# Performance work log

Hardware: AMD Instinct MI355X
Metric: run time of the kernel (lower is better)

## Reference

```python
import jax, jax.numpy as jnp
import numpy as np

N = 50000          # nodes
E = 800000         # edges per metapath
P = 4              # metapaths
IN = 256           # in_size
D = 32 * 8         # out_size * layer_num_heads = 256
SEM_H = 128        # SemanticAttention hidden


def setup_inputs() -> dict:
    key = jax.random.key(0)
    ks = jax.random.split(key, 8)
    h = jax.random.normal(ks[0], (N, IN), dtype=jnp.float32)
    src = jax.random.randint(ks[1], (P, E), 0, N, dtype=jnp.int32)
    dst = jax.random.randint(ks[2], (P, E), 0, N, dtype=jnp.int32)
    # per-metapath GraphConv weights (Glorot-ish scale)
    W_gc = jax.random.normal(ks[3], (P, IN, D), dtype=jnp.float32) / np.sqrt(IN)
    b_gc = jnp.zeros((P, D), dtype=jnp.float32)
    # SemanticAttention: Linear(D, SEM_H) -> tanh -> Linear(SEM_H, 1, bias=False)
    W1 = jax.random.normal(ks[4], (D, SEM_H), dtype=jnp.float32) / np.sqrt(D)
    b1 = jnp.zeros((SEM_H,), dtype=jnp.float32)
    w2 = jax.random.normal(ks[5], (SEM_H,), dtype=jnp.float32) / np.sqrt(SEM_H)
    return {"h": h, "src": src, "dst": dst, "W_gc": W_gc, "b_gc": b_gc,
            "W1": W1, "b1": b1, "w2": w2}


def _graph_conv(h, src, dst, W, b):
    # DGL GraphConv with norm='both': D_dst^{-1/2} A D_src^{-1/2} (h W) + b
    ones = jnp.ones((src.shape[0],), dtype=h.dtype)
    deg_out = jnp.clip(jax.ops.segment_sum(ones, src, num_segments=N), 1.0)
    deg_in = jnp.clip(jax.ops.segment_sum(ones, dst, num_segments=N), 1.0)
    x = (h @ W) * jax.lax.rsqrt(deg_out)[:, None]          # [N, D]
    agg = jax.ops.segment_sum(x[src], dst, num_segments=N)  # gather-scatter [N, D]
    return agg * jax.lax.rsqrt(deg_in)[:, None] + b


def reference(h, src, dst, W_gc, b_gc, W1, b1, w2):
    # per-metapath GraphConv (fixed small loop over P metapaths)
    zs = [_graph_conv(h, src[p], dst[p], W_gc[p], b_gc[p]) for p in range(P)]
    z = jnp.stack(zs, axis=1)                               # [N, P, D]
    # SemanticAttention: project -> mean over nodes -> softmax over metapaths
    s = jnp.tanh(z @ W1 + b1) @ w2                          # [N, P]
    beta = jax.nn.softmax(s.mean(axis=0), axis=0)           # [P]
    return jnp.einsum('npd,p->nd', z, beta)                 # [N, D]
```

## Files before the change

### kernel.cpp

```cpp
#include <hip/hip_runtime.h>

#define NN 50000
#define NE 800000
#define NP 4
#define DIN 256
#define DD 256
#define NH 128
#define SA 40
#define NSEG 16
#define SEGE (NE / NSEG)
#define HCH 16384
#define NHC 4
#define SCH 8192
#define NSC 7
#define SPAD(k) ((k) + ((k) >> 5))

typedef __attribute__((ext_vector_type(8))) short bf16x8;
typedef __attribute__((ext_vector_type(4))) float f32x4;
typedef __attribute__((ext_vector_type(2))) float f32x2;

__device__ __forceinline__ unsigned short f2bf(float f) {
  unsigned u = __float_as_uint(f);
  u += 0x7fff + ((u >> 16) & 1);
  return (unsigned short)(u >> 16);
}

__device__ __forceinline__ f32x2 unpk(unsigned u) {
  f32x2 f;
  f.x = __uint_as_float(u << 16);
  f.y = __uint_as_float(u & 0xffff0000u);
  return f;
}
__device__ __forceinline__ void pkfma(f32x2& acc, f32x2 m, f32x2 v) {
  asm("v_pk_fma_f32 %0, %1, %2, %0" : "+v"(acc) : "v"(m), "v"(v));
}


__global__ __launch_bounds__(256) void hist2d_kernel(const int* __restrict__ idx,
                                                     int* __restrict__ cnt) {
  int bx = blockIdx.x;
  int c = bx % NHC, s = bx / NHC;
  int p = blockIdx.y;
  int base = c * HCH, nk = min(HCH, NN - base);
  __shared__ int hs[HCH];
  for (int k = threadIdx.x; k < HCH; k += 256) hs[k] = 0;
  __syncthreads();
  const int4* a4 = (const int4*)(idx + (size_t)p * NE + (size_t)s * SEGE);
  for (int i = threadIdx.x; i < SEGE / 4; i += 256) {
    int4 v = a4[i];
    int k;
    k = v.x - base; if ((unsigned)k < (unsigned)nk) atomicAdd(&hs[k], 1);
    k = v.y - base; if ((unsigned)k < (unsigned)nk) atomicAdd(&hs[k], 1);
    k = v.z - base; if ((unsigned)k < (unsigned)nk) atomicAdd(&hs[k], 1);
    k = v.w - base; if ((unsigned)k < (unsigned)nk) atomicAdd(&hs[k], 1);
  }
  __syncthreads();
  int* out = cnt + (size_t)(p * NSEG + s) * NN + base;
  for (int k = threadIdx.x; k < nk; k += 256) out[k] = hs[k];
}


__global__ __launch_bounds__(1024) void scanA_kernel(
    int* __restrict__ cntD, const int* __restrict__ cntS,
    float* __restrict__ rin, float* __restrict__ rout,
    int* __restrict__ row_ptr, int* __restrict__ chunkdeg) {
  int c = blockIdx.x, p = blockIdx.y;
  int base = c * SCH, nk = min(SCH, NN - base);
  __shared__ int sdeg[SCH + (SCH >> 5)];
  __shared__ int wtot[16], wexc[16];
  int t = threadIdx.x;
  for (int kk = t; kk < SCH; kk += 1024) {
    int run = 0;
    if (kk < nk) {
      size_t o = (size_t)(p * NSEG) * NN + base + kk;
      for (int s = 0; s < NSEG; ++s) {
        size_t oo = o + (size_t)s * NN;
        int v = cntD[oo];
        cntD[oo] = run;
        run += v;
      }
      rin[(size_t)p * NN + base + kk] = rsqrtf((float)max(run, 1));
      int rs = 0;
      for (int s = 0; s < NSEG; ++s) rs += cntS[o + (size_t)s * NN];
      rout[(size_t)p * NN + base + kk] = rsqrtf((float)max(rs, 1));
    }
    sdeg[SPAD(kk)] = run;
  }
  __syncthreads();
  int loc[8];
  int ssum = 0;
#pragma unroll
  for (int j = 0; j < 8; ++j) { loc[j] = ssum; ssum += sdeg[SPAD(t * 8 + j)]; }
  int incl = ssum;
  int lane = t & 63, w = t >> 6;
#pragma unroll
  for (int o = 1; o < 64; o <<= 1) {
    int v = __shfl_up(incl, o);
    if (lane >= o) incl += v;
  }
  if (lane == 63) wtot[w] = incl;
  __syncthreads();
  if (t == 0) {
    int r = 0;
    for (int i = 0; i < 16; ++i) { wexc[i] = r; r += wtot[i]; }
  }
  __syncthreads();
  int tbase = wexc[w] + incl - ssum;
  int* rp = row_ptr + (size_t)p * (NN + 1) + base;
#pragma unroll
  for (int j = 0; j < 8; ++j) {
    int k = t * 8 + j;
    if (k < nk) rp[k] = tbase + loc[j];
  }
  if (t == 1023) chunkdeg[p * NSC + c] = tbase + ssum;
}


__global__ void scanB_kernel(const int* __restrict__ chunkdeg, int* __restrict__ chunk_base,
                             int* __restrict__ row_ptr) {
  int t = threadIdx.x;
  if (t < NP) {
    int run = 0;
    for (int c = 0; c < NSC; ++c) { chunk_base[t * NSC + c] = run; run += chunkdeg[t * NSC + c]; }
    row_ptr[(size_t)t * (NN + 1) + NN] = NE;
  }
}

__global__ __launch_bounds__(1024) void rpfin_kernel(int* __restrict__ row_ptr,
                                                     const int* __restrict__ chunk_base) {
  int k = blockIdx.x * 1024 + threadIdx.x, p = blockIdx.y;
  if (k < NN) row_ptr[(size_t)p * (NN + 1) + k] += chunk_base[p * NSC + (k >> 13)];
}


__global__ __launch_bounds__(256) void scatter_kernel(
    const int* __restrict__ src, const int* __restrict__ dst,
    const int* __restrict__ cntD, const int* __restrict__ row_ptr, int* __restrict__ col) {
  int bx = blockIdx.x;
  int c = bx % NHC, s = bx / NHC;
  int p = blockIdx.y;
  int base = c * HCH, nk = min(HCH, NN - base);
  __shared__ int cur[HCH];
  for (int k = threadIdx.x; k < nk; k += 256)
    cur[k] = row_ptr[(size_t)p * (NN + 1) + base + k] +
             cntD[(size_t)(p * NSEG + s) * NN + base + k];
  __syncthreads();
  const int4* d4 = (const int4*)(dst + (size_t)p * NE + (size_t)s * SEGE);
  const int4* s4 = (const int4*)(src + (size_t)p * NE + (size_t)s * SEGE);
  int* colp = col + (size_t)p * NE;
  for (int i = threadIdx.x; i < SEGE / 4; i += 256) {
    int4 dv = d4[i];
    int4 sv = s4[i];
    int k;
    k = dv.x - base; if ((unsigned)k < (unsigned)nk) colp[atomicAdd(&cur[k], 1)] = sv.x;
    k = dv.y - base; if ((unsigned)k < (unsigned)nk) colp[atomicAdd(&cur[k], 1)] = sv.y;
    k = dv.z - base; if ((unsigned)k < (unsigned)nk) colp[atomicAdd(&cur[k], 1)] = sv.z;
    k = dv.w - base; if ((unsigned)k < (unsigned)nk) colp[atomicAdd(&cur[k], 1)] = sv.w;
  }
}


__global__ void cvt_h_kernel(const float4* __restrict__ h4, ushort4* __restrict__ h2) {
  int i = blockIdx.x * blockDim.x + threadIdx.x;
  if (i >= NN * DIN / 4) return;
  float4 v = h4[i];
  ushort4 o;
  o.x = f2bf(v.x); o.y = f2bf(v.y); o.z = f2bf(v.z); o.w = f2bf(v.w);
  h2[i] = o;
}


__global__ __launch_bounds__(256) void agg_kernel(
    const ushort* __restrict__ h2, const int* __restrict__ col,
    const int* __restrict__ row_ptr, const float* __restrict__ rout,
    const float* __restrict__ rin, ushort* __restrict__ g) {
  __shared__ int2 sW[4][64];
  int p = blockIdx.y;
  int v = blockIdx.x * 4 + (threadIdx.x >> 6);
  int lane = threadIdx.x & 63;
  int wv = threadIdx.x >> 6;
  const int* colp = col + (size_t)p * NE;
  const float* rop = rout + (size_t)p * NN;
  int beg = row_ptr[p * (NN + 1) + v], end = row_ptr[p * (NN + 1) + v + 1];
  const char* hb = (const char*)h2 + (size_t)lane * 8;
  f32x2 accA0 = {0.f, 0.f}, accA1 = {0.f, 0.f};
  f32x2 accB0 = {0.f, 0.f}, accB1 = {0.f, 0.f};
  for (int j0 = beg; j0 < end; j0 += 64) {
    int nw = end - j0;
    if (nw > 64) nw = 64;
    int cv = 0;
    float rv = 0.f;
    if (lane < nw) { cv = colp[j0 + lane]; rv = rop[cv]; }
    sW[wv][lane] = make_int2(cv, __float_as_int(rv));
    int nwb = (nw + 7) & ~7;
    for (int t = 0; t < nwb; t += 8) {
      int2 w[8];
#pragma unroll
      for (int q = 0; q < 8; ++q) w[q] = sW[wv][t + q];
      uint2 u[8];
#pragma unroll
      for (int q = 0; q < 8; ++q)
        u[q] = *(const uint2*)(hb + ((size_t)(unsigned)w[q].x << 9));
#pragma unroll
      for (int q = 0; q < 8; ++q) {
        float r = __int_as_float(w[q].y);
        f32x2 rr = {r, r};
        if (q & 1) {
          pkfma(accB0, rr, unpk(u[q].x));
          pkfma(accB1, rr, unpk(u[q].y));
        } else {
          pkfma(accA0, rr, unpk(u[q].x));
          pkfma(accA1, rr, unpk(u[q].y));
        }
      }
    }
  }
  float ri = rin[(size_t)p * NN + v];
  f32x2 s0 = accA0 + accB0;
  f32x2 s1 = accA1 + accB1;
  ushort4 o;
  o.x = f2bf(s0.x * ri); o.y = f2bf(s0.y * ri);
  o.z = f2bf(s1.x * ri); o.w = f2bf(s1.y * ri);
  ((ushort4*)(g + ((size_t)p * NN + v) * DIN))[lane] = o;
}


__global__ void wmul_kernel(const float* __restrict__ Wgc, const float* __restrict__ W1,
                            ushort* __restrict__ Mt) {
  int p = blockIdx.y, k = blockIdx.x, j = threadIdx.x;
  const float* wrow = Wgc + ((size_t)p * DIN + k) * DD;
  float s = 0.f;
  for (int d = 0; d < DD; ++d) s = fmaf(wrow[d], W1[(size_t)d * NH + j], s);
  Mt[((size_t)p * NH + j) * DIN + k] = f2bf(s);
}

__global__ void cvec_kernel(const float* __restrict__ bgc, const float* __restrict__ W1,
                            const float* __restrict__ b1, float* __restrict__ cvec) {
  int p = blockIdx.x, j = threadIdx.x;
  const float* b = bgc + (size_t)p * DD;
  float s = b1[j];
  for (int d = 0; d < DD; ++d) s = fmaf(b[d], W1[(size_t)d * NH + j], s);
  cvec[p * NH + j] = s;
}


__global__ __launch_bounds__(256) void gemm_sem(
    const ushort* __restrict__ g, const ushort* __restrict__ Mt,
    const float* __restrict__ cvec, const float* __restrict__ w2,
    float* __restrict__ ssum) {
  __shared__ ushort As[128 * SA];
  __shared__ ushort Bs[128 * SA];
  __shared__ float wsumf[4];
  const int tid = threadIdx.x;
  const int p = blockIdx.y;
  const int row0 = blockIdx.x * 128;
  const int wave = tid >> 6, lane = tid & 63;
  const int wr = wave >> 1, wc = wave & 1;
  const int srow = tid >> 2, sseg = tid & 3;
  const int fr = lane & 15, fk = (lane >> 4) * 8;
  const ushort* Ag = g + (size_t)p * NN * DIN;
  const ushort* Bg = Mt + (size_t)p * NH * DIN;
  int ar0 = row0 + srow; if (ar0 >= NN) ar0 = NN - 1;
  int ar1 = row0 + srow + 64; if (ar1 >= NN) ar1 = NN - 1;
  f32x4 acc[4][4] = {};
  for (int k2 = 0; k2 < DIN; k2 += 32) {
    uint4 av0 = *(const uint4*)(Ag + (size_t)ar0 * DIN + k2 + sseg * 8);
    uint4 av1 = *(const uint4*)(Ag + (size_t)ar1 * DIN + k2 + sseg * 8);
    uint4 bv0 = *(const uint4*)(Bg + (size_t)srow * DIN + k2 + sseg * 8);
    uint4 bv1 = *(const uint4*)(Bg + (size_t)(srow + 64) * DIN + k2 + sseg * 8);
    __syncthreads();
    *(uint4*)&As[srow * SA + sseg * 8] = av0;
    *(uint4*)&As[(srow + 64) * SA + sseg * 8] = av1;
    *(uint4*)&Bs[srow * SA + sseg * 8] = bv0;
    *(uint4*)&Bs[(srow + 64) * SA + sseg * 8] = bv1;
    __syncthreads();
    bf16x8 af[4], bfv[4];
#pragma unroll
    for (int t = 0; t < 4; ++t) {
      af[t] = *(const bf16x8*)&As[(wr * 64 + t * 16 + fr) * SA + fk];
      bfv[t] = *(const bf16x8*)&Bs[(wc * 64 + t * 16 + fr) * SA + fk];
    }
#pragma unroll
    for (int mt = 0; mt < 4; ++mt)
#pragma unroll
      for (int nt = 0; nt < 4; ++nt)
        acc[mt][nt] = __builtin_amdgcn_mfma_f32_16x16x32_bf16(af[mt], bfv[nt], acc[mt][nt], 0, 0, 0);
  }
  float s = 0.f;
#pragma unroll
  for (int nt = 0; nt < 4; ++nt) {
    int c = wc * 64 + nt * 16 + fr;
    float cc = cvec[p * NH + c];
    float ww = w2[c];
#pragma unroll
    for (int mt = 0; mt < 4; ++mt)
#pragma unroll
      for (int i = 0; i < 4; ++i) {
        int r = row0 + wr * 64 + mt * 16 + (lane >> 4) * 4 + i;
        if (r < NN) {
          float x = acc[mt][nt][i] + cc;
          x = fminf(fmaxf(x, -15.f), 15.f);
          float e = __expf(2.f * x);
          s = fmaf((e - 1.f) / (e + 1.f), ww, s);
        }
      }
  }
#pragma unroll
  for (int o = 32; o > 0; o >>= 1) s += __shfl_down(s, o);
  if (lane == 0) wsumf[wave] = s;
  __syncthreads();
  if (tid == 0) atomicAdd(&ssum[p], wsumf[0] + wsumf[1] + wsumf[2] + wsumf[3]);
}


__global__ void beta_kernel(const float* __restrict__ ssum, const float* __restrict__ bgc,
                            float* __restrict__ beta, float* __restrict__ bout) {
  __shared__ float sb[NP];
  if (threadIdx.x == 0) {
    float m[NP];
    float mx = -1e30f;
    for (int p = 0; p < NP; ++p) {
      m[p] = ssum[p] / (float)NN;
      mx = fmaxf(mx, m[p]);
    }
    float tot = 0.f;
    for (int p = 0; p < NP; ++p) { m[p] = expf(m[p] - mx); tot += m[p]; }
    for (int p = 0; p < NP; ++p) { sb[p] = m[p] / tot; beta[p] = sb[p]; }
  }
  __syncthreads();
  int d = threadIdx.x;
  float s = 0.f;
  for (int p = 0; p < NP; ++p) s = fmaf(sb[p], bgc[p * DD + d], s);
  bout[d] = s;
}

__global__ void scaleWt_kernel(const float* __restrict__ Wgc, const float* __restrict__ beta,
                               ushort* __restrict__ Wt) {
  int i = blockIdx.x * blockDim.x + threadIdx.x;
  if (i >= DD * NP * DIN) return;
  int n = i >> 10;
  int pk = i & 1023;
  int p = pk >> 8, k = pk & 255;
  Wt[i] = f2bf(beta[p] * Wgc[((size_t)p * DIN + k) * DD + n]);
}


__global__ __launch_bounds__(256) void gemm_main(
    const ushort* __restrict__ g, const ushort* __restrict__ Wt,
    const float* __restrict__ bout, float* __restrict__ out) {
  __shared__ ushort As[128 * SA];
  __shared__ ushort Bs[128 * SA];
  const int tid = threadIdx.x;
  const int row0 = blockIdx.y * 128;
  const int col0 = blockIdx.x * 128;
  const int wave = tid >> 6, lane = tid & 63;
  const int wr = wave >> 1, wc = wave & 1;
  const int srow = tid >> 2, sseg = tid & 3;
  const int fr = lane & 15, fk = (lane >> 4) * 8;
  int ar0 = row0 + srow; if (ar0 >= NN) ar0 = NN - 1;
  int ar1 = row0 + srow + 64; if (ar1 >= NN) ar1 = NN - 1;
  f32x4 acc[4][4] = {};
  for (int p = 0; p < NP; ++p) {
    const ushort* Ag = g + (size_t)p * NN * DIN;
    for (int k2 = 0; k2 < DIN; k2 += 32) {
      uint4 av0 = *(const uint4*)(Ag + (size_t)ar0 * DIN + k2 + sseg * 8);
      uint4 av1 = *(const uint4*)(Ag + (size_t)ar1 * DIN + k2 + sseg * 8);
      uint4 bv0 = *(const uint4*)(Wt + (size_t)(col0 + srow) * (NP * DIN) + p * DIN + k2 + sseg * 8);
      uint4 bv1 = *(const uint4*)(Wt + (size_t)(col0 + srow + 64) * (NP * DIN) + p * DIN + k2 + sseg * 8);
      __syncthreads();
      *(uint4*)&As[srow * SA + sseg * 8] = av0;
      *(uint4*)&As[(srow + 64) * SA + sseg * 8] = av1;
      *(uint4*)&Bs[srow * SA + sseg * 8] = bv0;
      *(uint4*)&Bs[(srow + 64) * SA + sseg * 8] = bv1;
      __syncthreads();
      bf16x8 af[4], bfv[4];
#pragma unroll
      for (int t = 0; t < 4; ++t) {
        af[t] = *(const bf16x8*)&As[(wr * 64 + t * 16 + fr) * SA + fk];
        bfv[t] = *(const bf16x8*)&Bs[(wc * 64 + t * 16 + fr) * SA + fk];
      }
#pragma unroll
      for (int mt = 0; mt < 4; ++mt)
#pragma unroll
        for (int nt = 0; nt < 4; ++nt)
          acc[mt][nt] = __builtin_amdgcn_mfma_f32_16x16x32_bf16(af[mt], bfv[nt], acc[mt][nt], 0, 0, 0);
    }
  }
#pragma unroll
  for (int nt = 0; nt < 4; ++nt) {
    int c = col0 + wc * 64 + nt * 16 + fr;
    float bb = bout[c];
#pragma unroll
    for (int mt = 0; mt < 4; ++mt)
#pragma unroll
      for (int i = 0; i < 4; ++i) {
        int r = row0 + wr * 64 + mt * 16 + (lane >> 4) * 4 + i;
        if (r < NN) out[(size_t)r * DD + c] = acc[mt][nt][i] + bb;
      }
  }
}


extern "C" void kernel_launch(void* const* d_in, const int* in_sizes, int n_in,
                              void* d_out, int out_size, void* d_ws, size_t ws_size,
                              hipStream_t stream) {
  const float* h = (const float*)d_in[0];
  const int* src = (const int*)d_in[1];
  const int* dst = (const int*)d_in[2];
  const float* Wgc = (const float*)d_in[3];
  const float* bgc = (const float*)d_in[4];
  const float* W1 = (const float*)d_in[5];
  const float* b1 = (const float*)d_in[6];
  const float* w2 = (const float*)d_in[7];
  float* out = (float*)d_out;

  char* base = (char*)d_ws;
  size_t off = 0;
  auto alloc = [&](size_t bytes) -> char* {
    char* ptr = base + off;
    off = (off + bytes + 255) & ~(size_t)255;
    return ptr;
  };
  int* cntD = (int*)alloc((size_t)NP * NSEG * NN * sizeof(int));
  int* cntS = (int*)alloc((size_t)NP * NSEG * NN * sizeof(int));
  float* rin = (float*)alloc((size_t)NP * NN * sizeof(float));
  float* rout = (float*)alloc((size_t)NP * NN * sizeof(float));
  int* row_ptr = (int*)alloc((size_t)NP * (NN + 1) * sizeof(int));
  int* chunkdeg = (int*)alloc((size_t)NP * NSC * sizeof(int));
  int* chunk_base = (int*)alloc((size_t)NP * NSC * sizeof(int));
  ushort* h2 = (ushort*)alloc((size_t)NN * DIN * sizeof(ushort));
  ushort* g = (ushort*)alloc((size_t)NP * NN * DIN * sizeof(ushort));
  ushort* Mt = (ushort*)alloc((size_t)NP * NH * DIN * sizeof(ushort));
  ushort* Wt = (ushort*)alloc((size_t)DD * NP * DIN * sizeof(ushort));
  float* cvec = (float*)alloc((size_t)NP * NH * sizeof(float));
  float* ssum = (float*)alloc(NP * sizeof(float));
  float* beta = (float*)alloc(NP * sizeof(float));
  float* bout = (float*)alloc(DD * sizeof(float));
  int* colbuf = (int*)cntS;
  if (off > ws_size) return;

  hipMemsetAsync(ssum, 0, NP * sizeof(float), stream);

  hist2d_kernel<<<dim3(NHC * NSEG, NP), 256, 0, stream>>>(dst, cntD);
  hist2d_kernel<<<dim3(NHC * NSEG, NP), 256, 0, stream>>>(src, cntS);
  scanA_kernel<<<dim3(NSC, NP), 1024, 0, stream>>>(cntD, cntS, rin, rout, row_ptr, chunkdeg);
  scanB_kernel<<<1, 64, 0, stream>>>(chunkdeg, chunk_base, row_ptr);
  rpfin_kernel<<<dim3((NN + 1023) / 1024, NP), 1024, 0, stream>>>(row_ptr, chunk_base);
  cvt_h_kernel<<<(NN * DIN / 4 + 255) / 256, 256, 0, stream>>>((const float4*)h, (ushort4*)h2);
  scatter_kernel<<<dim3(NHC * NSEG, NP), 256, 0, stream>>>(src, dst, cntD, row_ptr, colbuf);
  agg_kernel<<<dim3(NN / 4, NP), 256, 0, stream>>>(h2, colbuf, row_ptr, rout, rin, g);
  wmul_kernel<<<dim3(DIN, NP), NH, 0, stream>>>(Wgc, W1, Mt);
  cvec_kernel<<<NP, NH, 0, stream>>>(bgc, W1, b1, cvec);
  gemm_sem<<<dim3((NN + 127) / 128, NP), 256, 0, stream>>>(g, Mt, cvec, w2, ssum);
  beta_kernel<<<1, 256, 0, stream>>>(ssum, bgc, beta, bout);
  scaleWt_kernel<<<(DD * NP * DIN + 255) / 256, 256, 0, stream>>>(Wgc, beta, Wt);
  gemm_main<<<dim3(2, (NN + 127) / 128), 256, 0, stream>>>(g, Wt, bout, out);
}
```

Baseline: 631.0 us.

## Precompute edge weights in CSR scatter and widen aggregation gathers to 16 bytes

The scatter kernel now stores each edge as an (src, rsqrt out-degree) pair, so the aggregation kernel no longer does a dependent gather of rout per edge. The aggregation kernel splits each wavefront into two halves that each process alternate edges, loading 16-byte rows per lane, and then combines the halves with a cross-lane shuffle. This removes one level of indirect loads and makes memory accesses wider. In exchange it needs an extra 8-byte-per-edge buffer instead of reusing cntS, does more random reads of rout in the scatter, and adds a shuffle reduction at the end.

```diff
diff --git a/kernel.cpp b/kernel.cpp
--- a/kernel.cpp
+++ b/kernel.cpp
@@ -23,6 +23,9 @@
   unsigned u = __float_as_uint(f);
   u += 0x7fff + ((u >> 16) & 1);
   return (unsigned short)(u >> 16);
+}
+__device__ __forceinline__ unsigned pk2(float a, float b) {
+  return (unsigned)f2bf(a) | ((unsigned)f2bf(b) << 16);
 }
 
 __device__ __forceinline__ f32x2 unpk(unsigned u) {
@@ -135,7 +138,8 @@
 
 __global__ __launch_bounds__(256) void scatter_kernel(
     const int* __restrict__ src, const int* __restrict__ dst,
-    const int* __restrict__ cntD, const int* __restrict__ row_ptr, int* __restrict__ col) {
+    const int* __restrict__ cntD, const int* __restrict__ row_ptr,
+    const float* __restrict__ rout, int2* __restrict__ col2) {
   int bx = blockIdx.x;
   int c = bx % NHC, s = bx / NHC;
   int p = blockIdx.y;
@@ -147,15 +151,32 @@
   __syncthreads();
   const int4* d4 = (const int4*)(dst + (size_t)p * NE + (size_t)s * SEGE);
   const int4* s4 = (const int4*)(src + (size_t)p * NE + (size_t)s * SEGE);
-  int* colp = col + (size_t)p * NE;
+  const float* rop = rout + (size_t)p * NN;
+  int2* colp = col2 + (size_t)p * NE;
   for (int i = threadIdx.x; i < SEGE / 4; i += 256) {
     int4 dv = d4[i];
     int4 sv = s4[i];
     int k;
-    k = dv.x - base; if ((unsigned)k < (unsigned)nk) colp[atomicAdd(&cur[k], 1)] = sv.x;
-    k = dv.y - base; if ((unsigned)k < (unsigned)nk) colp[atomicAdd(&cur[k], 1)] = sv.y;
-    k = dv.z - base; if ((unsigned)k < (unsigned)nk) colp[atomicAdd(&cur[k], 1)] = sv.z;
-    k = dv.w - base; if ((unsigned)k < (unsigned)nk) colp[atomicAdd(&cur[k], 1)] = sv.w;
+    k = dv.x - base;
+    if ((unsigned)k < (unsigned)nk) {
+      float wv = rop[sv.x];
+      colp[atomicAdd(&cur[k], 1)] = make_int2(sv.x, __float_as_int(wv));
+    }
+    k = dv.y - base;
+    if ((unsigned)k < (unsigned)nk) {
+      float wv = rop[sv.y];
+      colp[atomicAdd(&cur[k], 1)] = make_int2(sv.y, __float_as_int(wv));
+    }
+    k = dv.z - base;
+    if ((unsigned)k < (unsigned)nk) {
+      float wv = rop[sv.z];
+      colp[atomicAdd(&cur[k], 1)] = make_int2(sv.z, __float_as_int(wv));
+    }
+    k = dv.w - base;
+    if ((unsigned)k < (unsigned)nk) {
+      float wv = rop[sv.w];
+      colp[atomicAdd(&cur[k], 1)] = make_int2(sv.w, __float_as_int(wv));
+    }
   }
 }
 
@@ -171,57 +192,59 @@
 
 
 __global__ __launch_bounds__(256) void agg_kernel(
-    const ushort* __restrict__ h2, const int* __restrict__ col,
-    const int* __restrict__ row_ptr, const float* __restrict__ rout,
+    const ushort* __restrict__ h2, const int2* __restrict__ col2,
+    const int* __restrict__ row_ptr,
     const float* __restrict__ rin, ushort* __restrict__ g) {
   __shared__ int2 sW[4][64];
   int p = blockIdx.y;
   int v = blockIdx.x * 4 + (threadIdx.x >> 6);
   int lane = threadIdx.x & 63;
   int wv = threadIdx.x >> 6;
-  const int* colp = col + (size_t)p * NE;
-  const float* rop = rout + (size_t)p * NN;
+  const int2* colp = col2 + (size_t)p * NE;
   int beg = row_ptr[p * (NN + 1) + v], end = row_ptr[p * (NN + 1) + v + 1];
-  const char* hb = (const char*)h2 + (size_t)lane * 8;
-  f32x2 accA0 = {0.f, 0.f}, accA1 = {0.f, 0.f};
-  f32x2 accB0 = {0.f, 0.f}, accB1 = {0.f, 0.f};
+  const uint4* h4 = (const uint4*)h2;
+  int half = lane >> 5;
+  int l32 = lane & 31;
+  f32x2 acc0 = {0.f, 0.f}, acc1 = {0.f, 0.f}, acc2 = {0.f, 0.f}, acc3 = {0.f, 0.f};
   for (int j0 = beg; j0 < end; j0 += 64) {
     int nw = end - j0;
     if (nw > 64) nw = 64;
-    int cv = 0;
-    float rv = 0.f;
-    if (lane < nw) { cv = colp[j0 + lane]; rv = rop[cv]; }
-    sW[wv][lane] = make_int2(cv, __float_as_int(rv));
-    int nwb = (nw + 7) & ~7;
-    for (int t = 0; t < nwb; t += 8) {
+    int2 wp = make_int2(0, 0);
+    if (lane < nw) wp = colp[j0 + lane];
+    sW[wv][lane] = wp;
+    int nwb = (nw + 15) & ~15;
+    for (int t = 0; t < nwb; t += 16) {
       int2 w[8];
 #pragma unroll
-      for (int q = 0; q < 8; ++q) w[q] = sW[wv][t + q];
-      uint2 u[8];
+      for (int q = 0; q < 8; ++q) w[q] = sW[wv][t + 2 * q + half];
+      uint4 u[8];
 #pragma unroll
       for (int q = 0; q < 8; ++q)
-        u[q] = *(const uint2*)(hb + ((size_t)(unsigned)w[q].x << 9));
+        u[q] = h4[((unsigned)w[q].x << 5) + l32];
 #pragma unroll
       for (int q = 0; q < 8; ++q) {
         float r = __int_as_float(w[q].y);
         f32x2 rr = {r, r};
-        if (q & 1) {
-          pkfma(accB0, rr, unpk(u[q].x));
-          pkfma(accB1, rr, unpk(u[q].y));
-        } else {
-          pkfma(accA0, rr, unpk(u[q].x));
-          pkfma(accA1, rr, unpk(u[q].y));
-        }
+        pkfma(acc0, rr, unpk(u[q].x));
+        pkfma(acc1, rr, unpk(u[q].y));
+        pkfma(acc2, rr, unpk(u[q].z));
+        pkfma(acc3, rr, unpk(u[q].w));
       }
     }
   }
+  acc0.x += __shfl_xor(acc0.x, 32); acc0.y += __shfl_xor(acc0.y, 32);
+  acc1.x += __shfl_xor(acc1.x, 32); acc1.y += __shfl_xor(acc1.y, 32);
+  acc2.x += __shfl_xor(acc2.x, 32); acc2.y += __shfl_xor(acc2.y, 32);
+  acc3.x += __shfl_xor(acc3.x, 32); acc3.y += __shfl_xor(acc3.y, 32);
   float ri = rin[(size_t)p * NN + v];
-  f32x2 s0 = accA0 + accB0;
-  f32x2 s1 = accA1 + accB1;
-  ushort4 o;
-  o.x = f2bf(s0.x * ri); o.y = f2bf(s0.y * ri);
-  o.z = f2bf(s1.x * ri); o.w = f2bf(s1.y * ri);
-  ((ushort4*)(g + ((size_t)p * NN + v) * DIN))[lane] = o;
+  if (half == 0) {
+    uint4 o;
+    o.x = pk2(acc0.x * ri, acc0.y * ri);
+    o.y = pk2(acc1.x * ri, acc1.y * ri);
+    o.z = pk2(acc2.x * ri, acc2.y * ri);
+    o.w = pk2(acc3.x * ri, acc3.y * ri);
+    ((uint4*)(g + ((size_t)p * NN + v) * DIN))[l32] = o;
+  }
 }
 
 
@@ -436,7 +459,7 @@
   float* ssum = (float*)alloc(NP * sizeof(float));
   float* beta = (float*)alloc(NP * sizeof(float));
   float* bout = (float*)alloc(DD * sizeof(float));
-  int* colbuf = (int*)cntS;
+  int2* col2 = (int2*)alloc((size_t)NP * NE * sizeof(int2));
   if (off > ws_size) return;
 
   hipMemsetAsync(ssum, 0, NP * sizeof(float), stream);
@@ -447,8 +470,8 @@
   scanB_kernel<<<1, 64, 0, stream>>>(chunkdeg, chunk_base, row_ptr);
   rpfin_kernel<<<dim3((NN + 1023) / 1024, NP), 1024, 0, stream>>>(row_ptr, chunk_base);
   cvt_h_kernel<<<(NN * DIN / 4 + 255) / 256, 256, 0, stream>>>((const float4*)h, (ushort4*)h2);
-  scatter_kernel<<<dim3(NHC * NSEG, NP), 256, 0, stream>>>(src, dst, cntD, row_ptr, colbuf);
-  agg_kernel<<<dim3(NN / 4, NP), 256, 0, stream>>>(h2, colbuf, row_ptr, rout, rin, g);
+  scatter_kernel<<<dim3(NHC * NSEG, NP), 256, 0, stream>>>(src, dst, cntD, row_ptr, rout, col2);
+  agg_kernel<<<dim3(NN / 4, NP), 256, 0, stream>>>(h2, col2, row_ptr, rin, g);
   wmul_kernel<<<dim3(DIN, NP), NH, 0, stream>>>(Wgc, W1, Mt);
   cvec_kernel<<<NP, NH, 0, stream>>>(bgc, W1, b1, cvec);
   gemm_sem<<<dim3((NN + 127) / 128, NP), 256, 0, stream>>>(g, Mt, cvec, w2, ssum);
```

Measured after the change: 659.1 us. 1.04x slower.

## Widen main GEMM tile to full output width and fuse small setup kernels

Applied to the files above, without the earlier changes.

The main GEMM now has each block compute all 256 output columns for 128 rows, so the large g operand is read from memory once instead of twice. This doubles the accumulator registers per thread and the B tile in shared memory, which may reduce occupancy. The weight-product and bias-vector kernels are merged into one launch, and the softmax/beta step is folded into the weight scaling kernel, removing two launches. The aggregation inner loop is only rewritten inline with no change in behaviour.

```diff
diff --git a/kernel.cpp b/kernel.cpp
--- a/kernel.cpp
+++ b/kernel.cpp
@@ -24,16 +24,8 @@
   u += 0x7fff + ((u >> 16) & 1);
   return (unsigned short)(u >> 16);
 }
-
-__device__ __forceinline__ f32x2 unpk(unsigned u) {
-  f32x2 f;
-  f.x = __uint_as_float(u << 16);
-  f.y = __uint_as_float(u & 0xffff0000u);
-  return f;
-}
-__device__ __forceinline__ void pkfma(f32x2& acc, f32x2 m, f32x2 v) {
-  asm("v_pk_fma_f32 %0, %1, %2, %0" : "+v"(acc) : "v"(m), "v"(v));
-}
+__device__ __forceinline__ float bfl(unsigned u) { return __uint_as_float(u << 16); }
+__device__ __forceinline__ float bfh(unsigned u) { return __uint_as_float(u & 0xffff0000u); }
 
 
 __global__ __launch_bounds__(256) void hist2d_kernel(const int* __restrict__ idx,
@@ -206,11 +198,11 @@
         float r = __int_as_float(w[q].y);
         f32x2 rr = {r, r};
         if (q & 1) {
-          pkfma(accB0, rr, unpk(u[q].x));
-          pkfma(accB1, rr, unpk(u[q].y));
+          asm("v_pk_fma_f32 %0, %1, %2, %0" : "+v"(accB0) : "v"(rr), "v"((f32x2){bfl(u[q].x), bfh(u[q].x)}));
+          asm("v_pk_fma_f32 %0, %1, %2, %0" : "+v"(accB1) : "v"(rr), "v"((f32x2){bfl(u[q].y), bfh(u[q].y)}));
         } else {
-          pkfma(accA0, rr, unpk(u[q].x));
-          pkfma(accA1, rr, unpk(u[q].y));
+          asm("v_pk_fma_f32 %0, %1, %2, %0" : "+v"(accA0) : "v"(rr), "v"((f32x2){bfl(u[q].x), bfh(u[q].x)}));
+          asm("v_pk_fma_f32 %0, %1, %2, %0" : "+v"(accA1) : "v"(rr), "v"((f32x2){bfl(u[q].y), bfh(u[q].y)}));
         }
       }
     }
@@ -225,22 +217,21 @@
 }
 
 
-__global__ void wmul_kernel(const float* __restrict__ Wgc, const float* __restrict__ W1,
-                            ushort* __restrict__ Mt) {
+__global__ void wmulcvec_kernel(const float* __restrict__ Wgc, const float* __restrict__ bgc,
+                                const float* __restrict__ W1, const float* __restrict__ b1,
+                                ushort* __restrict__ Mt, float* __restrict__ cvec) {
   int p = blockIdx.y, k = blockIdx.x, j = threadIdx.x;
-  const float* wrow = Wgc + ((size_t)p * DIN + k) * DD;
-  float s = 0.f;
-  for (int d = 0; d < DD; ++d) s = fmaf(wrow[d], W1[(size_t)d * NH + j], s);
-  Mt[((size_t)p * NH + j) * DIN + k] = f2bf(s);
-}
-
-__global__ void cvec_kernel(const float* __restrict__ bgc, const float* __restrict__ W1,
-                            const float* __restrict__ b1, float* __restrict__ cvec) {
-  int p = blockIdx.x, j = threadIdx.x;
-  const float* b = bgc + (size_t)p * DD;
-  float s = b1[j];
-  for (int d = 0; d < DD; ++d) s = fmaf(b[d], W1[(size_t)d * NH + j], s);
-  cvec[p * NH + j] = s;
+  if (k < DIN) {
+    const float* wrow = Wgc + ((size_t)p * DIN + k) * DD;
+    float s = 0.f;
+    for (int d = 0; d < DD; ++d) s = fmaf(wrow[d], W1[(size_t)d * NH + j], s);
+    Mt[((size_t)p * NH + j) * DIN + k] = f2bf(s);
+  } else {
+    const float* b = bgc + (size_t)p * DD;
+    float s = b1[j];
+    for (int d = 0; d < DD; ++d) s = fmaf(b[d], W1[(size_t)d * NH + j], s);
+    cvec[p * NH + j] = s;
+  }
 }
 
 
@@ -313,35 +304,36 @@
 }
 
 
-__global__ void beta_kernel(const float* __restrict__ ssum, const float* __restrict__ bgc,
-                            float* __restrict__ beta, float* __restrict__ bout) {
-  __shared__ float sb[NP];
-  if (threadIdx.x == 0) {
-    float m[NP];
-    float mx = -1e30f;
-    for (int p = 0; p < NP; ++p) {
-      m[p] = ssum[p] / (float)NN;
-      mx = fmaxf(mx, m[p]);
-    }
-    float tot = 0.f;
-    for (int p = 0; p < NP; ++p) { m[p] = expf(m[p] - mx); tot += m[p]; }
-    for (int p = 0; p < NP; ++p) { sb[p] = m[p] / tot; beta[p] = sb[p]; }
-  }
-  __syncthreads();
-  int d = threadIdx.x;
-  float s = 0.f;
-  for (int p = 0; p < NP; ++p) s = fmaf(sb[p], bgc[p * DD + d], s);
-  bout[d] = s;
-}
-
-__global__ void scaleWt_kernel(const float* __restrict__ Wgc, const float* __restrict__ beta,
-                               ushort* __restrict__ Wt) {
-  int i = blockIdx.x * blockDim.x + threadIdx.x;
-  if (i >= DD * NP * DIN) return;
-  int n = i >> 10;
-  int pk = i & 1023;
-  int p = pk >> 8, k = pk & 255;
-  Wt[i] = f2bf(beta[p] * Wgc[((size_t)p * DIN + k) * DD + n]);
+__global__ __launch_bounds__(256) void scaleWtB_kernel(const float* __restrict__ Wgc,
+                                                       const float* __restrict__ ssum,
+                                                       const float* __restrict__ bgc,
+                                                       ushort* __restrict__ Wt,
+                                                       float* __restrict__ bout) {
+  float m[NP];
+  float mx = -1e30f;
+#pragma unroll
+  for (int p = 0; p < NP; ++p) {
+    m[p] = ssum[p] * (1.f / (float)NN);
+    mx = fmaxf(mx, m[p]);
+  }
+  float tot = 0.f;
+#pragma unroll
+  for (int p = 0; p < NP; ++p) { m[p] = __expf(m[p] - mx); tot += m[p]; }
+  float inv = 1.f / tot;
+  if (blockIdx.x == 0) {
+    int d = threadIdx.x;
+    float s = 0.f;
+#pragma unroll
+    for (int p = 0; p < NP; ++p) s = fmaf(m[p] * inv, bgc[p * DD + d], s);
+    bout[d] = s;
+  }
+  int i = blockIdx.x * 256 + threadIdx.x;
+  if (i < DD * NP * DIN) {
+    int n = i >> 10;
+    int pk = i & 1023;
+    int p = pk >> 8, k = pk & 255;
+    Wt[i] = f2bf(m[p] * inv * Wgc[((size_t)p * DIN + k) * DD + n]);
+  }
 }
 
 
@@ -349,46 +341,50 @@
     const ushort* __restrict__ g, const ushort* __restrict__ Wt,
     const float* __restrict__ bout, float* __restrict__ out) {
   __shared__ ushort As[128 * SA];
-  __shared__ ushort Bs[128 * SA];
+  __shared__ ushort Bs[256 * SA];
   const int tid = threadIdx.x;
-  const int row0 = blockIdx.y * 128;
-  const int col0 = blockIdx.x * 128;
+  const int row0 = blockIdx.x * 128;
   const int wave = tid >> 6, lane = tid & 63;
   const int wr = wave >> 1, wc = wave & 1;
   const int srow = tid >> 2, sseg = tid & 3;
   const int fr = lane & 15, fk = (lane >> 4) * 8;
   int ar0 = row0 + srow; if (ar0 >= NN) ar0 = NN - 1;
   int ar1 = row0 + srow + 64; if (ar1 >= NN) ar1 = NN - 1;
-  f32x4 acc[4][4] = {};
+  f32x4 acc[4][8] = {};
   for (int p = 0; p < NP; ++p) {
     const ushort* Ag = g + (size_t)p * NN * DIN;
     for (int k2 = 0; k2 < DIN; k2 += 32) {
       uint4 av0 = *(const uint4*)(Ag + (size_t)ar0 * DIN + k2 + sseg * 8);
       uint4 av1 = *(const uint4*)(Ag + (size_t)ar1 * DIN + k2 + sseg * 8);
-      uint4 bv0 = *(const uint4*)(Wt + (size_t)(col0 + srow) * (NP * DIN) + p * DIN + k2 + sseg * 8);
-      uint4 bv1 = *(const uint4*)(Wt + (size_t)(col0 + srow + 64) * (NP * DIN) + p * DIN + k2 + sseg * 8);
+      uint4 bv0 = *(const uint4*)(Wt + (size_t)srow * (NP * DIN) + p * DIN + k2 + sseg * 8);
+      uint4 bv1 = *(const uint4*)(Wt + (size_t)(srow + 64) * (NP * DIN) + p * DIN + k2 + sseg * 8);
+      uint4 bv2 = *(const uint4*)(Wt + (size_t)(srow + 128) * (NP * DIN) + p * DIN + k2 + sseg * 8);
+      uint4 bv3 = *(const uint4*)(Wt + (size_t)(srow + 192) * (NP * DIN) + p * DIN + k2 + sseg * 8);
       __syncthreads();
       *(uint4*)&As[srow * SA + sseg * 8] = av0;
       *(uint4*)&As[(srow + 64) * SA + sseg * 8] = av1;
       *(uint4*)&Bs[srow * SA + sseg * 8] = bv0;
       *(uint4*)&Bs[(srow + 64) * SA + sseg * 8] = bv1;
+      *(uint4*)&Bs[(srow + 128) * SA + sseg * 8] = bv2;
+      *(uint4*)&Bs[(srow + 192) * SA + sseg * 8] = bv3;
       __syncthreads();
-      bf16x8 af[4], bfv[4];
-#pragma unroll
-      for (int t = 0; t < 4; ++t) {
+      bf16x8 af[4], bfv[8];
+#pragma unroll
+      for (int t = 0; t < 4; ++t)
         af[t] = *(const bf16x8*)&As[(wr * 64 + t * 16 + fr) * SA + fk];
-        bfv[t] = *(const bf16x8*)&Bs[(wc * 64 + t * 16 + fr) * SA + fk];
-      }
+#pragma unroll
+      for (int nt = 0; nt < 8; ++nt)
+        bfv[nt] = *(const bf16x8*)&Bs[(wc * 128 + nt * 16 + fr) * SA + fk];
 #pragma unroll
       for (int mt = 0; mt < 4; ++mt)
 #pragma unroll
-        for (int nt = 0; nt < 4; ++nt)
+        for (int nt = 0; nt < 8; ++nt)
           acc[mt][nt] = __builtin_amdgcn_mfma_f32_16x16x32_bf16(af[mt], bfv[nt], acc[mt][nt], 0, 0, 0);
     }
   }
 #pragma unroll
-  for (int nt = 0; nt < 4; ++nt) {
-    int c = col0 + wc * 64 + nt * 16 + fr;
+  for (int nt = 0; nt < 8; ++nt) {
+    int c = wc * 128 + nt * 16 + fr;
     float bb = bout[c];
 #pragma unroll
     for (int mt = 0; mt < 4; ++mt)
@@ -434,7 +430,6 @@
   ushort* Wt = (ushort*)alloc((size_t)DD * NP * DIN * sizeof(ushort));
   float* cvec = (float*)alloc((size_t)NP * NH * sizeof(float));
   float* ssum = (float*)alloc(NP * sizeof(float));
-  float* beta = (float*)alloc(NP * sizeof(float));
   float* bout = (float*)alloc(DD * sizeof(float));
   int* colbuf = (int*)cntS;
   if (off > ws_size) return;
@@ -449,10 +444,8 @@
   cvt_h_kernel<<<(NN * DIN / 4 + 255) / 256, 256, 0, stream>>>((const float4*)h, (ushort4*)h2);
   scatter_kernel<<<dim3(NHC * NSEG, NP), 256, 0, stream>>>(src, dst, cntD, row_ptr, colbuf);
   agg_kernel<<<dim3(NN / 4, NP), 256, 0, stream>>>(h2, colbuf, row_ptr, rout, rin, g);
-  wmul_kernel<<<dim3(DIN, NP), NH, 0, stream>>>(Wgc, W1, Mt);
-  cvec_kernel<<<NP, NH, 0, stream>>>(bgc, W1, b1, cvec);
+  wmulcvec_kernel<<<dim3(DIN + 1, NP), NH, 0, stream>>>(Wgc, bgc, W1, b1, Mt, cvec);
   gemm_sem<<<dim3((NN + 127) / 128, NP), 256, 0, stream>>>(g, Mt, cvec, w2, ssum);
-  beta_kernel<<<1, 256, 0, stream>>>(ssum, bgc, beta, bout);
-  scaleWt_kernel<<<(DD * NP * DIN + 255) / 256, 256, 0, stream>>>(Wgc, beta, Wt);
-  gemm_main<<<dim3(2, (NN + 127) / 128), 256, 0, stream>>>(g, Wt, bout, out);
-}
+  scaleWtB_kernel<<<(DD * NP * DIN + 255) / 256, 256, 0, stream>>>(Wgc, ssum, bgc, Wt, bout);
+  gemm_main<<<dim3((NN + 127) / 128), 256, 0, stream>>>(g, Wt, bout, out);
+}
```

New measurement: 635.1 us. About the same (+0.6%).
